# Kernel tuning notes

Measured on AMD Instinct MI355X. Metric: run time of the kernel, lower is better.

## Reference

```python
import jax, jax.numpy as jnp
import numpy as np

D_MODEL, D_STATE, D_CONV, D_INNER = 1024, 16, 4, 2048
BATCH, SEQLEN = 4, 2048


def setup_inputs() -> dict:
    key = jax.random.key(0)
    ks = jax.random.split(key, 8)
    x = jax.random.normal(ks[0], (BATCH, SEQLEN, D_MODEL), jnp.float32)
    W_in = jax.random.normal(ks[1], (D_MODEL, 2 * D_INNER), jnp.float32) / np.float32(np.sqrt(D_MODEL))
    conv_w = jax.random.normal(ks[2], (D_INNER, 1, D_CONV), jnp.float32) * np.float32(0.3)
    W_x = jax.random.normal(ks[3], (D_INNER, 2 * D_STATE), jnp.float32) / np.float32(np.sqrt(D_INNER))
    W_dt = jax.random.normal(ks[4], (D_STATE, D_INNER), jnp.float32) / np.float32(np.sqrt(D_STATE))
    b_dt = jax.random.normal(ks[5], (D_INNER,), jnp.float32) * np.float32(0.1)
    W_Bp = jax.random.normal(ks[6], (D_STATE, D_INNER), jnp.float32) / np.float32(np.sqrt(D_STATE))
    D_param = jnp.ones((D_INNER,), jnp.float32)
    W_out = jax.random.normal(ks[7], (D_INNER, D_MODEL), jnp.float32) / np.float32(np.sqrt(D_INNER))
    return {"x": x, "W_in": W_in, "conv_w": conv_w, "W_x": W_x,
            "W_dt": W_dt, "b_dt": b_dt, "W_Bp": W_Bp, "D_param": D_param,
            "W_out": W_out}


def _mamba_fwd(x, W_in, conv_w, W_x, W_dt, b_dt, W_Bp, D_param, W_out):
    B, L, _ = x.shape
    xz = x @ W_in                                   # [B,L,2*d_inner]
    xc, z = jnp.split(xz, 2, axis=-1)
    # causal depthwise conv1d (torch pads d_conv-1 both sides then slices [:L])
    xt = jnp.transpose(xc, (0, 2, 1))               # [B,d_inner,L]
    xt = jax.lax.conv_general_dilated(
        xt, conv_w,
        window_strides=(1,), padding=[(D_CONV - 1, 0)],
        dimension_numbers=("NCH", "OIH", "NCH"),
        feature_group_count=D_INNER)
    u = jax.nn.silu(jnp.transpose(xt, (0, 2, 1)))   # [B,L,d_inner]
    xp = u @ W_x                                    # [B,L,2*d_state]
    dt_raw, B_raw = jnp.split(xp, 2, axis=-1)
    dt = jax.nn.softplus(dt_raw @ W_dt + b_dt)      # [B,L,d_inner]
    Bp = B_raw @ W_Bp                               # [B,L,d_inner]
    dt = jnp.clip(dt, 1e-4, 1.0)
    # selective scan: h_t = h_{t-1}*(1-dt_t) + u_t*Bp_t (note: A is unused in source)
    ub = u * Bp
    def step(h, inp):
        d_t, ub_t = inp
        h = h * (1.0 - d_t) + ub_t
        return h, h
    _, ys = jax.lax.scan(step, jnp.zeros((B, D_INNER), x.dtype),
                         (jnp.transpose(dt, (1, 0, 2)), jnp.transpose(ub, (1, 0, 2))))
    y = jnp.transpose(ys, (1, 0, 2)) + D_param * u  # [B,L,d_inner]
    y = y * jax.nn.silu(z)
    return y @ W_out                                # [B,L,d_model]


def reference(x, W_in, conv_w, W_x, W_dt, b_dt, W_Bp, D_param, W_out):
    # dropout is identity in eval mode
    return _mamba_fwd(x, W_in, conv_w, W_x, W_dt, b_dt, W_Bp, D_param, W_out)
```

## Files before the change

kernel.cpp:

```cpp
#include <hip/hip_runtime.h>
#include <cstdint>
#include <cstddef>

#define DM   1024
#define DI   2048
#define SEQ  2048
#define NB   4
#define NTOK (NB*SEQ)
#define CCH  32
#define LC   (SEQ/CCH)
#define KS   8

typedef __attribute__((ext_vector_type(8))) short short8v;
typedef __attribute__((ext_vector_type(4))) float f32x4;
typedef unsigned short u16;
typedef unsigned int   u32;

__device__ __forceinline__ float silu_f(float x){ return x / (1.f + __expf(-x)); }

__device__ __forceinline__ float softplus_f(float x){
  return (x > 20.f) ? x : __logf(1.f + __expf(x));
}

__device__ __forceinline__ u16 f2bf(float f){
  union { float f; u32 u; } c; c.f = f;
  u32 u = c.u + 0x7FFFu + ((c.u >> 16) & 1u);
  return (u16)(u >> 16);
}
__device__ __forceinline__ float b2f(u16 b){
  union { u32 u; float f; } c; c.u = ((u32)b) << 16; return c.f;
}
__device__ __forceinline__ float lo2f(u32 v){ union { u32 u; float f; } c; c.u = v << 16; return c.f; }
__device__ __forceinline__ float hi2f(u32 v){ union { u32 u; float f; } c; c.u = v & 0xFFFF0000u; return c.f; }
__device__ __forceinline__ u32 pack2(float a, float b){ return (u32)f2bf(a) | ((u32)f2bf(b) << 16); }

__device__ __forceinline__ void gl16(const void* g, void* l){
  __builtin_amdgcn_global_load_lds((const __attribute__((address_space(1))) void*)g,
                                   (__attribute__((address_space(3))) void*)l, 16, 0, 0);
}

#define PREP_CVT   8192
#define PREP_T1    (PREP_CVT + 1024)
#define PREP_T2    (PREP_T1 + 512)
#define PREP_TOTAL (PREP_T2 + 768)

__device__ void transcvt_dev(const float* __restrict__ W, u16* __restrict__ Wt,
                             int R, int Cn, int bx, int by, int tid,
                             float (*t)[65])
{
  const int lr4 = tid >> 6;
  const int lc  = tid & 63;
  #pragma unroll
  for (int p = 0; p < 16; ++p) {
    int lr = p * 4 + lr4;
    t[lr][lc] = W[(size_t)(by * 64 + lr) * Cn + bx * 64 + lc];
  }
  __syncthreads();
  #pragma unroll
  for (int p = 0; p < 16; ++p) {
    int orr = p * 4 + lr4;
    Wt[(size_t)(bx * 64 + orr) * R + by * 64 + lc] = f2bf(t[lc][orr]);
  }
}

__global__ __launch_bounds__(256) void prep_all(
    const float* __restrict__ x, u16* __restrict__ xbf,
    const float* __restrict__ W_in, u16* __restrict__ wtib,
    const float* __restrict__ W_out, u16* __restrict__ wtob,
    const float* __restrict__ W_x, const float* __restrict__ W_dt,
    const float* __restrict__ W_Bp, u16* __restrict__ Wxt, u16* __restrict__ Wbig)
{
  __shared__ float t[64][65];
  const int bid = blockIdx.x, tid = threadIdx.x;
  if (bid < PREP_CVT) {
    int i = bid * 256 + tid;
    float4 v = ((const float4*)x)[i];
    *(uint2*)(xbf + (size_t)i * 4) = make_uint2(pack2(v.x, v.y), pack2(v.z, v.w));
  } else if (bid < PREP_T1) {
    int r = bid - PREP_CVT;
    transcvt_dev(W_in, wtib, DM, 2 * DI, r & 63, r >> 6, tid, t);
  } else if (bid < PREP_T2) {
    int r = bid - PREP_T1;
    transcvt_dev(W_out, wtob, DI, DM, r & 15, r >> 4, tid, t);
  } else {
    int i = (bid - PREP_T2) * 256 + tid;
    if (i < 32 * DI) {
      int j = i >> 11, c = i & (DI - 1);
      Wxt[i] = f2bf(W_x[c * 32 + j]);
    }
    int i2 = i - 32 * DI;
    if (i2 >= 0 && i2 < 2 * DI * 32) {
      int n = i2 >> 5, k = i2 & 31;
      float v;
      if (n < DI) v = (k < 16) ? W_dt[k * DI + n] : 0.f;
      else        v = (k >= 16) ? W_Bp[(k - 16) * DI + (n - DI)] : 0.f;
      Wbig[i2] = f2bf(v);
    }
  }
}

template<int NT, int OBF16>
__global__ __launch_bounds__(256, 2) void gemm2b(
    const u16* __restrict__ A, const u16* __restrict__ Bt,
    void* C0v, void* C1v, int K, int split, int ldc)
{
  __shared__ __align__(16) u16 Ab[2][128 * 64];
  __shared__ __align__(16) u16 Bb[2][128 * 64];
  const int tid = threadIdx.x, lane = tid & 63, w = tid >> 6;
  const int wm = w >> 1, wn = w & 1;
  const int bm = blockIdx.y * 128, bn = blockIdx.x * 128;

  const int srow8 = tid >> 3;
  const int kc = ((tid & 7) ^ (srow8 & 7)) << 3;
  const u16* Ag = A  + (size_t)(bm + srow8) * K + kc;
  const u16* Bg = Bt + (size_t)(bn + srow8) * K + kc;

  const int lq = lane >> 4, l15 = lane & 15;
  const int co0 = ((lq    ) ^ (l15 & 7)) << 3;
  const int co1 = ((lq + 4) ^ (l15 & 7)) << 3;
  const int abase = (wm * 64 + l15) * 64;
  const int bbase = (wn * 64 + l15) * 64;

  f32x4 acc[4][4] = {};

  auto issue = [&](int t, int buf) {
    const size_t k0 = (size_t)t << 6;
    #pragma unroll
    for (int q = 0; q < 4; ++q)
      gl16(Ag + (size_t)(q * 32) * K + k0, &Ab[buf][q * 2048 + tid * 8]);
    #pragma unroll
    for (int q = 0; q < 4; ++q)
      gl16(Bg + (size_t)(q * 32) * K + k0, &Bb[buf][q * 2048 + tid * 8]);
  };
  auto compute = [&](int buf) {
    const u16* Ac = Ab[buf];
    const u16* Bc = Bb[buf];
    short8v af[4], bf[4];
    #pragma unroll
    for (int ks = 0; ks < 2; ++ks) {
      const int co = ks ? co1 : co0;
      #pragma unroll
      for (int i = 0; i < 4; ++i) af[i] = *(const short8v*)&Ac[abase + i * 1024 + co];
      #pragma unroll
      for (int j = 0; j < 4; ++j) bf[j] = *(const short8v*)&Bc[bbase + j * 1024 + co];
      __builtin_amdgcn_s_setprio(1);
      #pragma unroll
      for (int i = 0; i < 4; ++i)
        #pragma unroll
        for (int j = 0; j < 4; ++j)
          acc[i][j] = __builtin_amdgcn_mfma_f32_16x16x32_bf16(af[i], bf[j], acc[i][j], 0, 0, 0);
      __builtin_amdgcn_s_setprio(0);
    }
  };

  issue(0, 0); issue(1, 1);
  #pragma unroll 1
  for (int t = 0; t < NT; ++t) {
    if (t + 1 < NT) asm volatile("s_waitcnt vmcnt(8)" ::: "memory");
    else            asm volatile("s_waitcnt vmcnt(0)" ::: "memory");
    __builtin_amdgcn_s_barrier(); __builtin_amdgcn_sched_barrier(0);
    compute(t & 1);
    __builtin_amdgcn_s_barrier(); __builtin_amdgcn_sched_barrier(0);
    if (t + 2 < NT) issue(t + 2, t & 1);
  }

  const bool left = (bn < split);
  const int cb = bn - (left ? 0 : split) + wn * 64 + l15;
  const int rb = bm + wm * 64 + lq * 4;
  if (OBF16) {
    u16* Cp = (u16*)(left ? C0v : C1v);
    #pragma unroll
    for (int i = 0; i < 4; ++i)
      #pragma unroll
      for (int j = 0; j < 4; ++j)
        #pragma unroll
        for (int r = 0; r < 4; ++r)
          Cp[(size_t)(rb + i * 16 + r) * ldc + cb + j * 16] = f2bf(acc[i][j][r]);
  } else {
    float* Cp = (float*)(left ? C0v : C1v);
    #pragma unroll
    for (int i = 0; i < 4; ++i)
      #pragma unroll
      for (int j = 0; j < 4; ++j)
        #pragma unroll
        for (int r = 0; r < 4; ++r)
          Cp[(size_t)(rb + i * 16 + r) * ldc + cb + j * 16] = acc[i][j][r];
  }
}

__global__ __launch_bounds__(256) void xp_gemm(
    const u16* __restrict__ A, const u16* __restrict__ Bt, float* __restrict__ xpp)
{
  __shared__ __align__(16) u16 Asm[128 * 32];
  __shared__ __align__(16) u16 Bsm[32 * 32];
  const int tid = threadIdx.x, lane = tid & 63, w = tid >> 6;
  const int bm = blockIdx.x * 128;
  const int kbase = blockIdx.y * (DI / KS);
  f32x4 acc[2][2] = {};
  const int srow = w * 32 + (lane >> 2);
  const int soct = lane & 3;
  const u16* Ap = A + (size_t)(bm + srow) * DI + kbase + soct * 8;
  const u16* Bp = Bt + (size_t)(lane >> 2) * DI + kbase + soct * 8;
  u16* As0 = &Asm[w * 1024];

  for (int k0 = 0; k0 < DI / KS; k0 += 32) {
    gl16(Ap + k0,                      As0);
    gl16(Ap + k0 + (size_t)16 * DI,    As0 + 512);
    if (w == 0) {
      gl16(Bp + k0,                    Bsm);
      gl16(Bp + k0 + (size_t)16 * DI,  Bsm + 512);
    }
    __syncthreads();
    short8v af[2], bf[2];
    #pragma unroll
    for (int i = 0; i < 2; ++i)
      af[i] = *(const short8v*)&Asm[(w * 32 + i * 16 + (lane & 15)) * 32 + (lane >> 4) * 8];
    #pragma unroll
    for (int j = 0; j < 2; ++j)
      bf[j] = *(const short8v*)&Bsm[(j * 16 + (lane & 15)) * 32 + (lane >> 4) * 8];
    #pragma unroll
    for (int i = 0; i < 2; ++i)
      #pragma unroll
      for (int j = 0; j < 2; ++j)
        acc[i][j] = __builtin_amdgcn_mfma_f32_16x16x32_bf16(af[i], bf[j], acc[i][j], 0, 0, 0);
    __syncthreads();
  }
  float* op = xpp + (size_t)blockIdx.y * NTOK * 32;
  const int rb = bm + w * 32 + (lane >> 4) * 4;
  const int cb = lane & 15;
  #pragma unroll
  for (int i = 0; i < 2; ++i)
    #pragma unroll
    for (int j = 0; j < 2; ++j)
      #pragma unroll
      for (int r = 0; r < 4; ++r)
        op[(size_t)(rb + i * 16 + r) * 32 + cb + j * 16] = acc[i][j][r];
}

__global__ __launch_bounds__(256) void xp_reduce(
    const float* __restrict__ xpp, u16* __restrict__ xpb)
{
  int i = blockIdx.x * 256 + threadIdx.x;
  float s = 0.f;
  #pragma unroll
  for (int k = 0; k < KS; ++k) s += xpp[(size_t)k * NTOK * 32 + i];
  xpb[i] = f2bf(s);
}

__global__ __launch_bounds__(256) void dtub_gemm(
    const u16* __restrict__ A, const u16* __restrict__ Bt,
    const float* __restrict__ b_dt, const u16* __restrict__ u,
    u16* __restrict__ dt_out, u16* __restrict__ ub_out)
{
  __shared__ __align__(16) u16 Asm[128 * 32];
  __shared__ __align__(16) u16 Bsm[128 * 32];
  const int tid = threadIdx.x, lane = tid & 63, w = tid >> 6;
  const int wm = w >> 1, wn = w & 1;
  const int bm = blockIdx.y * 128, bn = blockIdx.x * 128;
  const int srow = w * 32 + (lane >> 2);
  const int soct = lane & 3;
  u16* As0 = &Asm[w * 1024];
  u16* Bs0 = &Bsm[w * 1024];
  gl16(A  + (size_t)(bm + srow) * 32 + soct * 8,       As0);
  gl16(A  + (size_t)(bm + srow) * 32 + soct * 8 + 512, As0 + 512);
  gl16(Bt + (size_t)(bn + srow) * 32 + soct * 8,       Bs0);
  gl16(Bt + (size_t)(bn + srow) * 32 + soct * 8 + 512, Bs0 + 512);
  __syncthreads();
  f32x4 acc[4][4] = {};
  short8v afr[4], bfr[4];
  #pragma unroll
  for (int i = 0; i < 4; ++i) {
    afr[i] = *(const short8v*)&Asm[(wm * 64 + i * 16 + (lane & 15)) * 32 + (lane >> 4) * 8];
    bfr[i] = *(const short8v*)&Bsm[(wn * 64 + i * 16 + (lane & 15)) * 32 + (lane >> 4) * 8];
  }
  #pragma unroll
  for (int i = 0; i < 4; ++i)
    #pragma unroll
    for (int j = 0; j < 4; ++j)
      acc[i][j] = __builtin_amdgcn_mfma_f32_16x16x32_bf16(afr[i], bfr[j], acc[i][j], 0, 0, 0);

  const int rb = bm + wm * 64 + (lane >> 4) * 4;
  const int cb = bn + wn * 64 + (lane & 15);
  if (bn < DI) {
    float bd[4];
    #pragma unroll
    for (int j = 0; j < 4; ++j) bd[j] = b_dt[cb + j * 16];
    #pragma unroll
    for (int i = 0; i < 4; ++i)
      #pragma unroll
      for (int j = 0; j < 4; ++j)
        #pragma unroll
        for (int r = 0; r < 4; ++r) {
          float sp = softplus_f(acc[i][j][r] + bd[j]);
          sp = fminf(fmaxf(sp, 1e-4f), 1.0f);
          dt_out[(size_t)(rb + i * 16 + r) * DI + cb + j * 16] = f2bf(sp);
        }
  } else {
    const int cn = cb - DI;
    #pragma unroll
    for (int i = 0; i < 4; ++i)
      #pragma unroll
      for (int j = 0; j < 4; ++j)
        #pragma unroll
        for (int r = 0; r < 4; ++r) {
          size_t off = (size_t)(rb + i * 16 + r) * DI + cn + j * 16;
          ub_out[off] = f2bf(b2f(u[off]) * acc[i][j][r]);
        }
  }
}

__global__ __launch_bounds__(256) void conv_silu_k(
    const u16* __restrict__ xc, const float* __restrict__ cw, u16* __restrict__ u)
{
  int idx = blockIdx.x * 256 + threadIdx.x;
  int c = (idx & (DI / 4 - 1)) << 2;
  int r = idx >> 9;
  int t = r & (SEQ - 1);
  float4 w0 = ((const float4*)cw)[c + 0];
  float4 w1 = ((const float4*)cw)[c + 1];
  float4 w2 = ((const float4*)cw)[c + 2];
  float4 w3 = ((const float4*)cw)[c + 3];
  const u16* base = xc + (size_t)r * DI + c;
  uint2 v = *(const uint2*)base;
  float a0 = w0.w * lo2f(v.x), a1 = w1.w * hi2f(v.x);
  float a2 = w2.w * lo2f(v.y), a3 = w3.w * hi2f(v.y);
  if (t >= 1) { v = *(const uint2*)(base - DI);
    a0 += w0.z * lo2f(v.x); a1 += w1.z * hi2f(v.x); a2 += w2.z * lo2f(v.y); a3 += w3.z * hi2f(v.y); }
  if (t >= 2) { v = *(const uint2*)(base - 2 * DI);
    a0 += w0.y * lo2f(v.x); a1 += w1.y * hi2f(v.x); a2 += w2.y * lo2f(v.y); a3 += w3.y * hi2f(v.y); }
  if (t >= 3) { v = *(const uint2*)(base - 3 * DI);
    a0 += w0.x * lo2f(v.x); a1 += w1.x * hi2f(v.x); a2 += w2.x * lo2f(v.y); a3 += w3.x * hi2f(v.y); }
  *(uint2*)(u + (size_t)r * DI + c) =
      make_uint2(pack2(silu_f(a0), silu_f(a1)), pack2(silu_f(a2), silu_f(a3)));
}

__global__ __launch_bounds__(256) void scan_p1(
    const u16* __restrict__ dt_, const u16* __restrict__ ub,
    float* __restrict__ P, float* __restrict__ S)
{
  int idx = blockIdx.x * 256 + threadIdx.x;
  int di = (idx & (DI / 4 - 1)) << 2;
  int bc = idx >> 9;
  int c  = bc & (CCH - 1);
  int b  = bc >> 5;
  size_t base = ((size_t)b * SEQ + (size_t)c * LC) * DI + di;
  float p0 = 1.f, s0 = 0.f, p1 = 1.f, s1 = 0.f;
  float p2 = 1.f, s2 = 0.f, p3 = 1.f, s3 = 0.f;
  #pragma unroll 4
  for (int t = 0; t < LC; ++t) {
    size_t off = base + (size_t)t * DI;
    uint2 dv = *(const uint2*)(dt_ + off);
    uint2 uv = *(const uint2*)(ub + off);
    float a0 = 1.f - lo2f(dv.x), a1 = 1.f - hi2f(dv.x);
    float a2 = 1.f - lo2f(dv.y), a3 = 1.f - hi2f(dv.y);
    s0 = s0 * a0 + lo2f(uv.x); p0 *= a0;
    s1 = s1 * a1 + hi2f(uv.x); p1 *= a1;
    s2 = s2 * a2 + lo2f(uv.y); p2 *= a2;
    s3 = s3 * a3 + hi2f(uv.y); p3 *= a3;
  }
  ((float4*)P)[idx] = make_float4(p0, p1, p2, p3);
  ((float4*)S)[idx] = make_float4(s0, s1, s2, s3);
}

__global__ __launch_bounds__(256) void scan_p2(
    const float* __restrict__ P, const float* __restrict__ S, float* __restrict__ Hin)
{
  int idx = blockIdx.x * 256 + threadIdx.x;
  int di = idx & (DI - 1);
  int b  = idx >> 11;
  float h = 0.f;
  #pragma unroll
  for (int c = 0; c < CCH; ++c) {
    size_t off = ((size_t)b * CCH + c) * DI + di;
    Hin[off] = h;
    h = h * P[off] + S[off];
  }
}

__global__ __launch_bounds__(256) void scan_p3(
    const u16* dt_, const u16* __restrict__ ub, const u16* __restrict__ u,
    const u16* __restrict__ z, const float* __restrict__ Dp_,
    const float* __restrict__ Hin, u16* y)
{
  int idx = blockIdx.x * 256 + threadIdx.x;
  int di = (idx & (DI / 4 - 1)) << 2;
  int bc = idx >> 9;
  int c  = bc & (CCH - 1);
  int b  = bc >> 5;
  float4 dp = ((const float4*)Dp_)[di >> 2];
  float4 h4 = ((const float4*)Hin)[idx];
  float h0 = h4.x, h1 = h4.y, h2 = h4.z, h3 = h4.w;
  size_t base = ((size_t)b * SEQ + (size_t)c * LC) * DI + di;
  #pragma unroll 4
  for (int t = 0; t < LC; ++t) {
    size_t off = base + (size_t)t * DI;
    uint2 dv = *(const uint2*)(dt_ + off);
    uint2 uv = *(const uint2*)(ub + off);
    uint2 uu = *(const uint2*)(u + off);
    uint2 zv = *(const uint2*)(z + off);
    h0 = h0 * (1.f - lo2f(dv.x)) + lo2f(uv.x);
    h1 = h1 * (1.f - hi2f(dv.x)) + hi2f(uv.x);
    h2 = h2 * (1.f - lo2f(dv.y)) + lo2f(uv.y);
    h3 = h3 * (1.f - hi2f(dv.y)) + hi2f(uv.y);
    float y0 = (h0 + dp.x * lo2f(uu.x)) * silu_f(lo2f(zv.x));
    float y1 = (h1 + dp.y * hi2f(uu.x)) * silu_f(hi2f(zv.x));
    float y2 = (h2 + dp.z * lo2f(uu.y)) * silu_f(lo2f(zv.y));
    float y3 = (h3 + dp.w * hi2f(uu.y)) * silu_f(hi2f(zv.y));
    *(uint2*)(y + off) = make_uint2(pack2(y0, y1), pack2(y2, y3));
  }
}

extern "C" void kernel_launch(void* const* d_in, const int* in_sizes, int n_in,
                              void* d_out, int out_size, void* d_ws, size_t ws_size,
                              hipStream_t stream)
{
  const float* x     = (const float*)d_in[0];
  const float* W_in  = (const float*)d_in[1];
  const float* cw    = (const float*)d_in[2];
  const float* W_x   = (const float*)d_in[3];
  const float* W_dt  = (const float*)d_in[4];
  const float* b_dt  = (const float*)d_in[5];
  const float* W_Bp  = (const float*)d_in[6];
  const float* Dp    = (const float*)d_in[7];
  const float* W_out = (const float*)d_in[8];
  float* out = (float*)d_out;

  const size_t SZ = (size_t)NTOK * DI;
  float* w    = (float*)d_ws;
  float* bufA = w;
  float* bufB = w + SZ;
  float* bufC = w + 2 * SZ;
  float* bufD = w + 3 * SZ;

  u16* xcb  = (u16*)bufA;
  u16* zb   = (u16*)bufB;
  u16* wtob = zb + (size_t)NTOK * DI;
  u16* wxt  = wtob + (size_t)DM * DI;
  u16* wbig = wxt + (size_t)32 * DI;
  u16* xbf  = (u16*)bufC;
  u16* wtib = xbf + (size_t)NTOK * DM;
  u16* ubf  = (u16*)bufC;
  u16* ubb  = (u16*)bufD;

  const size_t PS = (size_t)NB * CCH * DI;
  float* Pbuf   = out;
  float* Sbuf   = out + PS;
  float* Hin    = out + 2 * PS;
  float* xppart = out + 3 * PS;
  u16*   xpb    = (u16*)(out + 3 * PS + (size_t)KS * NTOK * 32);
  (void)ws_size; (void)in_sizes; (void)n_in; (void)out_size;

  prep_all<<<PREP_TOTAL, 256, 0, stream>>>(
      x, xbf, W_in, wtib, W_out, wtob, W_x, W_dt, W_Bp, wxt, wbig);

  gemm2b<DM / 64, 1><<<dim3((2 * DI) / 128, NTOK / 128), 256, 0, stream>>>(
      xbf, wtib, (void*)xcb, (void*)zb, DM, DI, DI);

  conv_silu_k<<<(NTOK * DI / 4) / 256, 256, 0, stream>>>(xcb, cw, ubf);

  xp_gemm<<<dim3(NTOK / 128, KS), 256, 0, stream>>>(ubf, wxt, xppart);
  xp_reduce<<<(NTOK * 32) / 256, 256, 0, stream>>>(xppart, xpb);
  dtub_gemm<<<dim3((2 * DI) / 128, NTOK / 128), 256, 0, stream>>>(
      xpb, wbig, b_dt, ubf, xcb, ubb);

  scan_p1<<<(NB * CCH * DI / 4) / 256, 256, 0, stream>>>(xcb, ubb, Pbuf, Sbuf);
  scan_p2<<<(NB * DI) / 256, 256, 0, stream>>>(Pbuf, Sbuf, Hin);
  scan_p3<<<(NB * CCH * DI / 4) / 256, 256, 0, stream>>>(xcb, ubb, ubf, zb, Dp, Hin, xcb);

  gemm2b<DI / 64, 0><<<dim3(DM / 128, NTOK / 128), 256, 0, stream>>>(
      xcb, wtob, (void*)out, (void*)out, DI, DM, DM);
}
```

Measured before the change: 293.0 us.

## Fuse dt/ub projection GEMM with chunk-level scan pass one

Each block now computes both the dt and ub tiles for the same 128 columns, so u is paired with both projections at once. The results are staged in LDS, and the per-chunk scan products and sums (P, S) are computed there directly from 64-row chunks. This removes the separate scan_p1 kernel and its global re-read of dt and ub. It costs a larger 64KB LDS footprint and longer per-block serial work, which may reduce occupancy.

```diff
diff --git a/kernel.cpp b/kernel.cpp
--- a/kernel.cpp
+++ b/kernel.cpp
@@ -247,65 +247,87 @@
   xpb[i] = f2bf(s);
 }
 
-__global__ __launch_bounds__(256) void dtub_gemm(
-    const u16* __restrict__ A, const u16* __restrict__ Bt,
+__global__ __launch_bounds__(256) void dtub_scan(
+    const u16* __restrict__ A,
+    const u16* __restrict__ Bt,
     const float* __restrict__ b_dt, const u16* __restrict__ u,
-    u16* __restrict__ dt_out, u16* __restrict__ ub_out)
-{
-  __shared__ __align__(16) u16 Asm[128 * 32];
-  __shared__ __align__(16) u16 Bsm[128 * 32];
+    u16* __restrict__ dt_out, u16* __restrict__ ub_out,
+    float* __restrict__ P, float* __restrict__ S)
+{
+  __shared__ __align__(16) u16 smem[32768];
+  u16* Asm = smem;
+  u16* Bsm = smem + 4096;
   const int tid = threadIdx.x, lane = tid & 63, w = tid >> 6;
   const int wm = w >> 1, wn = w & 1;
-  const int bm = blockIdx.y * 128, bn = blockIdx.x * 128;
+  const int bm = blockIdx.y * 128, bc = blockIdx.x * 128;
   const int srow = w * 32 + (lane >> 2);
   const int soct = lane & 3;
-  u16* As0 = &Asm[w * 1024];
-  u16* Bs0 = &Bsm[w * 1024];
-  gl16(A  + (size_t)(bm + srow) * 32 + soct * 8,       As0);
-  gl16(A  + (size_t)(bm + srow) * 32 + soct * 8 + 512, As0 + 512);
-  gl16(Bt + (size_t)(bn + srow) * 32 + soct * 8,       Bs0);
-  gl16(Bt + (size_t)(bn + srow) * 32 + soct * 8 + 512, Bs0 + 512);
+  u16* As0 = Asm + w * 1024;
+  u16* Bs0 = Bsm + w * 1024;
+  u16* Bs1 = Bsm + 4096 + w * 1024;
+  gl16(A  + (size_t)(bm + srow) * 32 + soct * 8,            As0);
+  gl16(A  + (size_t)(bm + srow) * 32 + soct * 8 + 512,      As0 + 512);
+  gl16(Bt + (size_t)(bc + srow) * 32 + soct * 8,            Bs0);
+  gl16(Bt + (size_t)(bc + srow) * 32 + soct * 8 + 512,      Bs0 + 512);
+  gl16(Bt + (size_t)(DI + bc + srow) * 32 + soct * 8,       Bs1);
+  gl16(Bt + (size_t)(DI + bc + srow) * 32 + soct * 8 + 512, Bs1 + 512);
   __syncthreads();
-  f32x4 acc[4][4] = {};
-  short8v afr[4], bfr[4];
+
+  const int lq = lane >> 4, l15 = lane & 15;
+  f32x4 accd[4][4] = {}, accu[4][4] = {};
+  short8v afr[4], bfd[4], bfu[4];
   #pragma unroll
   for (int i = 0; i < 4; ++i) {
-    afr[i] = *(const short8v*)&Asm[(wm * 64 + i * 16 + (lane & 15)) * 32 + (lane >> 4) * 8];
-    bfr[i] = *(const short8v*)&Bsm[(wn * 64 + i * 16 + (lane & 15)) * 32 + (lane >> 4) * 8];
+    afr[i] = *(const short8v*)&Asm[(wm * 64 + i * 16 + l15) * 32 + lq * 8];
+    bfd[i] = *(const short8v*)&Bsm[(wn * 64 + i * 16 + l15) * 32 + lq * 8];
+    bfu[i] = *(const short8v*)&Bsm[4096 + (wn * 64 + i * 16 + l15) * 32 + lq * 8];
   }
   #pragma unroll
   for (int i = 0; i < 4; ++i)
     #pragma unroll
+    for (int j = 0; j < 4; ++j) {
+      accd[i][j] = __builtin_amdgcn_mfma_f32_16x16x32_bf16(afr[i], bfd[j], accd[i][j], 0, 0, 0);
+      accu[i][j] = __builtin_amdgcn_mfma_f32_16x16x32_bf16(afr[i], bfu[j], accu[i][j], 0, 0, 0);
+    }
+  __syncthreads();
+  u16* dtL = smem;
+  u16* ubL = smem + 16384;
+
+  const int rl = wm * 64 + lq * 4;
+  const int cl = wn * 64 + l15;
+  float bd[4];
+  #pragma unroll
+  for (int j = 0; j < 4; ++j) bd[j] = b_dt[bc + cl + j * 16];
+  #pragma unroll
+  for (int i = 0; i < 4; ++i)
+    #pragma unroll
     for (int j = 0; j < 4; ++j)
-      acc[i][j] = __builtin_amdgcn_mfma_f32_16x16x32_bf16(afr[i], bfr[j], acc[i][j], 0, 0, 0);
-
-  const int rb = bm + wm * 64 + (lane >> 4) * 4;
-  const int cb = bn + wn * 64 + (lane & 15);
-  if (bn < DI) {
-    float bd[4];
-    #pragma unroll
-    for (int j = 0; j < 4; ++j) bd[j] = b_dt[cb + j * 16];
-    #pragma unroll
-    for (int i = 0; i < 4; ++i)
-      #pragma unroll
-      for (int j = 0; j < 4; ++j)
-        #pragma unroll
-        for (int r = 0; r < 4; ++r) {
-          float sp = softplus_f(acc[i][j][r] + bd[j]);
-          sp = fminf(fmaxf(sp, 1e-4f), 1.0f);
-          dt_out[(size_t)(rb + i * 16 + r) * DI + cb + j * 16] = f2bf(sp);
-        }
-  } else {
-    const int cn = cb - DI;
-    #pragma unroll
-    for (int i = 0; i < 4; ++i)
-      #pragma unroll
-      for (int j = 0; j < 4; ++j)
-        #pragma unroll
-        for (int r = 0; r < 4; ++r) {
-          size_t off = (size_t)(rb + i * 16 + r) * DI + cn + j * 16;
-          ub_out[off] = f2bf(b2f(u[off]) * acc[i][j][r]);
-        }
+      #pragma unroll
+      for (int r = 0; r < 4; ++r) {
+        const int row = rl + i * 16 + r, col = cl + j * 16;
+        const size_t off = (size_t)(bm + row) * DI + bc + col;
+        float sp = softplus_f(accd[i][j][r] + bd[j]);
+        sp = fminf(fmaxf(sp, 1e-4f), 1.0f);
+        u16 dv = f2bf(sp);
+        u16 uv = f2bf(b2f(u[off]) * accu[i][j][r]);
+        dt_out[off] = dv; dtL[row * 128 + col] = dv;
+        ub_out[off] = uv; ubL[row * 128 + col] = uv;
+      }
+  __syncthreads();
+
+  {
+    const int chunk = tid >> 7, ch = tid & 127;
+    float p = 1.f, s = 0.f;
+    #pragma unroll 4
+    for (int t = 0; t < LC; ++t) {
+      int rr = chunk * LC + t;
+      float a = 1.f - b2f(dtL[rr * 128 + ch]);
+      s = s * a + b2f(ubL[rr * 128 + ch]);
+      p *= a;
+    }
+    const int gt = (bm >> 6) + chunk;
+    P[(size_t)gt * DI + bc + ch] = p;
+    S[(size_t)gt * DI + bc + ch] = s;
   }
 }
 
@@ -332,34 +354,6 @@
     a0 += w0.x * lo2f(v.x); a1 += w1.x * hi2f(v.x); a2 += w2.x * lo2f(v.y); a3 += w3.x * hi2f(v.y); }
   *(uint2*)(u + (size_t)r * DI + c) =
       make_uint2(pack2(silu_f(a0), silu_f(a1)), pack2(silu_f(a2), silu_f(a3)));
-}
-
-__global__ __launch_bounds__(256) void scan_p1(
-    const u16* __restrict__ dt_, const u16* __restrict__ ub,
-    float* __restrict__ P, float* __restrict__ S)
-{
-  int idx = blockIdx.x * 256 + threadIdx.x;
-  int di = (idx & (DI / 4 - 1)) << 2;
-  int bc = idx >> 9;
-  int c  = bc & (CCH - 1);
-  int b  = bc >> 5;
-  size_t base = ((size_t)b * SEQ + (size_t)c * LC) * DI + di;
-  float p0 = 1.f, s0 = 0.f, p1 = 1.f, s1 = 0.f;
-  float p2 = 1.f, s2 = 0.f, p3 = 1.f, s3 = 0.f;
-  #pragma unroll 4
-  for (int t = 0; t < LC; ++t) {
-    size_t off = base + (size_t)t * DI;
-    uint2 dv = *(const uint2*)(dt_ + off);
-    uint2 uv = *(const uint2*)(ub + off);
-    float a0 = 1.f - lo2f(dv.x), a1 = 1.f - hi2f(dv.x);
-    float a2 = 1.f - lo2f(dv.y), a3 = 1.f - hi2f(dv.y);
-    s0 = s0 * a0 + lo2f(uv.x); p0 *= a0;
-    s1 = s1 * a1 + hi2f(uv.x); p1 *= a1;
-    s2 = s2 * a2 + lo2f(uv.y); p2 *= a2;
-    s3 = s3 * a3 + hi2f(uv.y); p3 *= a3;
-  }
-  ((float4*)P)[idx] = make_float4(p0, p1, p2, p3);
-  ((float4*)S)[idx] = make_float4(s0, s1, s2, s3);
 }
 
 __global__ __launch_bounds__(256) void scan_p2(
@@ -460,10 +454,9 @@
 
   xp_gemm<<<dim3(NTOK / 128, KS), 256, 0, stream>>>(ubf, wxt, xppart);
   xp_reduce<<<(NTOK * 32) / 256, 256, 0, stream>>>(xppart, xpb);
-  dtub_gemm<<<dim3((2 * DI) / 128, NTOK / 128), 256, 0, stream>>>(
-      xpb, wbig, b_dt, ubf, xcb, ubb);
-
-  scan_p1<<<(NB * CCH * DI / 4) / 256, 256, 0, stream>>>(xcb, ubb, Pbuf, Sbuf);
+  dtub_scan<<<dim3(DI / 128, NTOK / 128), 256, 0, stream>>>(
+      xpb, wbig, b_dt, ubf, xcb, ubb, Pbuf, Sbuf);
+
   scan_p2<<<(NB * DI) / 256, 256, 0, stream>>>(Pbuf, Sbuf, Hin);
   scan_p3<<<(NB * CCH * DI / 4) / 256, 256, 0, stream>>>(xcb, ubb, ubf, zb, Dp, Hin, xcb);
 
```

After: 281.5 us, median of 2. 3.9% less time.
